# Kernel tuning notes

Measured on AMD Instinct MI355X. Metric: run time of the kernel, lower is better.

The kernel has to match this reference:

```python
import jax, jax.numpy as jnp
import numpy as np

D_MODEL = 768
N_HEADS = 8
HEAD_DIM = D_MODEL // N_HEADS  # 96


def setup_inputs() -> dict:
    key = jax.random.key(0)
    k1, k2, k3, k4, k5 = jax.random.split(key, 5)
    B, LQ, LK = 2, 4096, 4096
    hidden_states = jax.random.normal(k1, (B, LQ, D_MODEL), dtype=jnp.float32)
    key_value_states = jax.random.normal(k2, (B, LK, D_MODEL), dtype=jnp.float32)
    # learned projection params (initialized as eye in torch, but learned; use random here)
    Wq = jax.random.normal(k3, (D_MODEL, D_MODEL), dtype=jnp.float32) * 0.02
    Wk = jax.random.normal(k4, (D_MODEL, D_MODEL), dtype=jnp.float32) * 0.02
    Wv = jax.random.normal(k5, (D_MODEL, D_MODEL), dtype=jnp.float32) * 0.02
    return {"hidden_states": hidden_states, "key_value_states": key_value_states,
            "Wq": Wq, "Wk": Wk, "Wv": Wv}


def reference(hidden_states, key_value_states, Wq, Wk, Wv):
    B, LQ, _ = hidden_states.shape
    LK = key_value_states.shape[1]
    # linear projections (no bias)
    q = hidden_states @ Wq            # [B, LQ, D]
    k = key_value_states @ Wk         # [B, LK, D]
    v = key_value_states @ Wv         # [B, LK, D]
    # split heads: [B, H, L, d]
    def shape(x, L):
        return x.reshape(B, L, N_HEADS, HEAD_DIM).transpose(0, 2, 1, 3)
    q = shape(q, LQ) / jnp.sqrt(jnp.float32(HEAD_DIM))
    k = shape(k, LK)
    v = shape(v, LK)
    scores = jnp.einsum('bhqd,bhkd->bhqk', q, k)   # [B, H, LQ, LK]
    attn = jax.nn.softmax(scores, axis=-1)
    # dropout p=0.0 -> identity
    ctx = jnp.einsum('bhqk,bhkd->bhqd', attn, v)   # [B, H, LQ, d]
    context = ctx.transpose(0, 2, 1, 3).reshape(B, LQ, D_MODEL)
    return context
```

## Files before the change

kernel.cpp:

```cpp
#include <hip/hip_runtime.h>
#include <hip/hip_bf16.h>


typedef __bf16 bf16x8 __attribute__((ext_vector_type(8)));
typedef __bf16 bf16x4 __attribute__((ext_vector_type(4)));
typedef float  f32x4  __attribute__((ext_vector_type(4)));
typedef float  f32x16 __attribute__((ext_vector_type(16)));
typedef unsigned u32x4 __attribute__((ext_vector_type(4)));

#define DM   768
#define NH   8
#define HD   96
#define SEQ  4096
#define BATCH 2
#define WELEM (DM*DM)
#define XELEM (BATCH*SEQ*DM)

#define GLDS16(gp, lp) __builtin_amdgcn_global_load_lds( \
    (const __attribute__((address_space(1))) void*)(gp), \
    (__attribute__((address_space(3))) void*)(lp), 16, 0, 0)

__global__ __launch_bounds__(256) void transpose_w3(
    const float* __restrict__ Wq, const float* __restrict__ Wk, const float* __restrict__ Wv,
    __bf16* __restrict__ Tq, __bf16* __restrict__ Tk, __bf16* __restrict__ Tv)
{
    __shared__ __bf16 Ls[64][72];
    const int id = blockIdx.x;
    const int which = id / 144;
    const int tile = id - which * 144;
    const int ti = tile / 12, tj = tile % 12;
    const float* W = (which == 0) ? Wq : (which == 1) ? Wk : Wv;
    __bf16* T      = (which == 0) ? Tq : (which == 1) ? Tk : Tv;

    const int t = threadIdx.x;
    const int row = t >> 2, q4 = t & 3;
    const float* src = W + (size_t)(ti * 64 + row) * DM + tj * 64 + q4 * 16;
    float4 f0 = *reinterpret_cast<const float4*>(src);
    float4 f1 = *reinterpret_cast<const float4*>(src + 4);
    float4 f2 = *reinterpret_cast<const float4*>(src + 8);
    float4 f3 = *reinterpret_cast<const float4*>(src + 12);
    bf16x8 v0, v1;
    v0[0]=(__bf16)f0.x; v0[1]=(__bf16)f0.y; v0[2]=(__bf16)f0.z; v0[3]=(__bf16)f0.w;
    v0[4]=(__bf16)f1.x; v0[5]=(__bf16)f1.y; v0[6]=(__bf16)f1.z; v0[7]=(__bf16)f1.w;
    v1[0]=(__bf16)f2.x; v1[1]=(__bf16)f2.y; v1[2]=(__bf16)f2.z; v1[3]=(__bf16)f2.w;
    v1[4]=(__bf16)f3.x; v1[5]=(__bf16)f3.y; v1[6]=(__bf16)f3.z; v1[7]=(__bf16)f3.w;
    *reinterpret_cast<bf16x8*>(&Ls[row][q4 * 16])     = v0;
    *reinterpret_cast<bf16x8*>(&Ls[row][q4 * 16 + 8]) = v1;
    __syncthreads();
    #pragma unroll
    for (int j = 0; j < 2; ++j) {
        const int idx = t + j * 256;
        const int orow = idx >> 3, oc = idx & 7;
        bf16x8 o;
        #pragma unroll
        for (int e = 0; e < 8; ++e) o[e] = Ls[oc * 8 + e][orow];
        *reinterpret_cast<bf16x8*>(
            &T[(size_t)(tj * 64 + orow) * DM + ti * 64 + oc * 8]) = o;
    }
}

__global__ __launch_bounds__(256) void convert_x(
    const float* __restrict__ X0, const float* __restrict__ X1,
    __bf16* __restrict__ Y0, __bf16* __restrict__ Y1)
{
    const float* X = blockIdx.y ? X1 : X0;
    __bf16* Y      = blockIdx.y ? Y1 : Y0;
    const size_t i = ((size_t)blockIdx.x * 256 + threadIdx.x) * 8;
    float4 lo = *reinterpret_cast<const float4*>(X + i);
    float4 hi = *reinterpret_cast<const float4*>(X + i + 4);
    bf16x8 v;
    v[0]=(__bf16)lo.x; v[1]=(__bf16)lo.y; v[2]=(__bf16)lo.z; v[3]=(__bf16)lo.w;
    v[4]=(__bf16)hi.x; v[5]=(__bf16)hi.y; v[6]=(__bf16)hi.z; v[7]=(__bf16)hi.w;
    *reinterpret_cast<bf16x8*>(Y + i) = v;
}

__global__ __launch_bounds__(256, 2) void proj_all(
    const __bf16* __restrict__ Xh, const __bf16* __restrict__ Xkv,
    const __bf16* __restrict__ Wtq, const __bf16* __restrict__ Wtk,
    const __bf16* __restrict__ Wtv, __bf16* __restrict__ Yq,
    __bf16* __restrict__ Yk, __bf16* __restrict__ Yv, float qscale)
{
    __shared__ __bf16 As[2][128][64];
    __shared__ __bf16 Bs[2][128][64];

    const int t = threadIdx.x;
    const int l = t & 63;
    const int w = t >> 6;
    const int ln = l & 15, g = l >> 4;
    const int wm = w >> 1, wn = w & 1;

    const int id3 = blockIdx.x;
    const int xcd = id3 & 7;
    const int u = id3 >> 3;
    const int which = u % 3;
    const int c = u / 3;
    const int m0 = (xcd * 8 + c / 6) * 128;
    const int n0 = (c % 6) * 128;

    const __bf16* Xb = (which == 0) ? Xh : Xkv;
    const __bf16* Wt = (which == 0) ? Wtq : (which == 1) ? Wtk : Wtv;
    __bf16* Y        = (which == 0) ? Yq : (which == 1) ? Yk : Yv;
    const int mode   = (which == 2) ? 1 : 0;
    const float scale = (which == 0) ? qscale : 1.0f;

    size_t asrc[4], bsrc[4]; unsigned sdst[4];
    #pragma unroll
    for (int j = 0; j < 4; ++j) {
        const int cid = j * 256 + t;
        const int r = cid >> 3, cc = cid & 7, cs = cc ^ (r & 7);
        asrc[j] = (size_t)(m0 + r) * DM + cs * 8;
        bsrc[j] = (size_t)(n0 + r) * DM + cs * 8;
        sdst[j] = cid * 16;
    }

    f32x4 acc[4][4] = {};

    #pragma unroll
    for (int j = 0; j < 4; ++j) GLDS16(Xb + asrc[j], (char*)As + sdst[j]);
    #pragma unroll
    for (int j = 0; j < 4; ++j) GLDS16(Wt + bsrc[j], (char*)Bs + sdst[j]);
    __syncthreads();

    const int NKT = DM / 64;
    for (int kt = 0; kt < NKT; ++kt) {
        const int cur = kt & 1;
        if (kt + 1 < NKT) {
            const unsigned nb = (cur ^ 1) * 16384u;
            const size_t k0n = (size_t)(kt + 1) * 64;
            #pragma unroll
            for (int j = 0; j < 4; ++j) GLDS16(Xb + k0n + asrc[j], (char*)As + nb + sdst[j]);
            #pragma unroll
            for (int j = 0; j < 4; ++j) GLDS16(Wt + k0n + bsrc[j], (char*)Bs + nb + sdst[j]);
        }

        #pragma unroll
        for (int kk = 0; kk < 2; ++kk) {
            bf16x8 a[4], b[4];
            #pragma unroll
            for (int ms = 0; ms < 4; ++ms) {
                const int row = wm * 64 + ms * 16 + ln;
                const int slot = (kk * 4 + g) ^ (row & 7);
                a[ms] = *reinterpret_cast<const bf16x8*>(
                    (const char*)As + cur * 16384 + row * 128 + slot * 16);
            }
            #pragma unroll
            for (int ns = 0; ns < 4; ++ns) {
                const int row = wn * 64 + ns * 16 + ln;
                const int slot = (kk * 4 + g) ^ (row & 7);
                b[ns] = *reinterpret_cast<const bf16x8*>(
                    (const char*)Bs + cur * 16384 + row * 128 + slot * 16);
            }
            #pragma unroll
            for (int ms = 0; ms < 4; ++ms)
                #pragma unroll
                for (int ns = 0; ns < 4; ++ns)
                    acc[ms][ns] = __builtin_amdgcn_mfma_f32_16x16x32_bf16(
                        a[ms], b[ns], acc[ms][ns], 0, 0, 0);
        }
        __syncthreads();
    }

    #pragma unroll
    for (int ms = 0; ms < 4; ++ms) {
        #pragma unroll
        for (int ns = 0; ns < 4; ++ns) {
            const int col = n0 + wn * 64 + ns * 16 + ln;
            const int h = col / HD, d = col - h * HD;
            const int row_base = m0 + wm * 64 + ms * 16 + 4 * g;
            if (mode == 0) {
                #pragma unroll
                for (int r = 0; r < 4; ++r) {
                    const int row = row_base + r;
                    const int b_ = row >> 12, q = row & (SEQ - 1);
                    Y[(((size_t)(b_ * NH + h) * SEQ) + q) * HD + d] =
                        (__bf16)(acc[ms][ns][r] * scale);
                }
            } else {
                const int b_ = row_base >> 12, kq = row_base & (SEQ - 1);
                bf16x4 v;
                #pragma unroll
                for (int r = 0; r < 4; ++r) v[r] = (__bf16)acc[ms][ns][r];
                *reinterpret_cast<bf16x4*>(
                    &Y[((size_t)(b_ * NH + h) * HD + d) * SEQ + kq]) = v;
            }
        }
    }
}

__global__ __launch_bounds__(256, 2) void attn_kernel(
    const __bf16* __restrict__ Q, const __bf16* __restrict__ K,
    const __bf16* __restrict__ Vt, float* __restrict__ out)
{
    __shared__ __bf16 Ks[2][64][128];
    __shared__ __bf16 Vs[3][96][64];

    const int t_ = threadIdx.x;
    const int l = t_ & 63;
    const int w = t_ >> 6;
    const int lh = l >> 5;
    const int c31 = l & 31;

    const int swz = (blockIdx.x & 7) * 64 + (blockIdx.x >> 3);
    const int bh = swz >> 5;
    const int qb = swz & 31;
    const int b = bh >> 3, hd = bh & 7;
    const int q0 = qb * 128 + w * 32;

    const size_t base = (size_t)bh * SEQ * HD;
    const __bf16* Kg = K + base;
    const __bf16* Vg = Vt + base;

    size_t ksrc[4], vsrc[3];
    unsigned kdst[4], vdst[3];
    #pragma unroll
    for (int j = 0; j < 4; ++j) {
        const int cid = (w * 4 + j) * 64 + l;
        const int r = cid >> 4, cc = cid & 15;
        int cs = cc ^ (r & 7); if (cs >= 12) cs = 0;
        ksrc[j] = (size_t)r * HD + cs * 8;
        kdst[j] = (w * 4 + j) * 1024;
    }
    #pragma unroll
    for (int j = 0; j < 3; ++j) {
        const int cid = (w * 3 + j) * 64 + l;
        const int d = cid >> 3, cc = cid & 7;
        const int cs = cc ^ (d & 7);
        vsrc[j] = (size_t)d * SEQ + cs * 8;
        vdst[j] = (w * 3 + j) * 1024;
    }

    bf16x8 qf[6];
    #pragma unroll
    for (int st = 0; st < 6; ++st)
        qf[st] = *reinterpret_cast<const bf16x8*>(
            &Q[base + (size_t)(q0 + c31) * HD + st * 16 + 8 * lh]);

    f32x16 acc[3] = {};
    f32x16 sA0, sA1, sB0, sB1;
    float l_r = 0.f;
    int vcur = 0, vst = 2;
    f32x16 ZC = {};
    asm volatile("" : "+v"(ZC));

    auto STAGE = [&](int tile, int kp, int vbuf) {
        const size_t ko = (size_t)tile * 64 * HD;
        #pragma unroll
        for (int j = 0; j < 4; ++j)
            GLDS16(Kg + ko + ksrc[j], (char*)Ks + kp * 16384 + kdst[j]);
        const size_t vo = (size_t)tile * 64;
        #pragma unroll
        for (int j = 0; j < 3; ++j)
            GLDS16(Vg + vo + vsrc[j], (char*)Vs + vbuf * 12288 + vdst[j]);
    };

    auto QKT = [&](int pbuf, f32x16& S0, f32x16& S1) {
        #pragma unroll
        for (int st = 0; st < 6; ++st) {
            const int slot = (2 * st + lh) ^ (c31 & 7);
            bf16x8 ka0 = *reinterpret_cast<const bf16x8*>(
                (const char*)Ks + pbuf * 16384 + c31 * 256 + slot * 16);
            bf16x8 ka1 = *reinterpret_cast<const bf16x8*>(
                (const char*)Ks + pbuf * 16384 + (32 + c31) * 256 + slot * 16);
            S0 = __builtin_amdgcn_mfma_f32_32x32x16_bf16(ka0, qf[st],
                     st == 0 ? ZC : S0, 0, 0, 0);
            S1 = __builtin_amdgcn_mfma_f32_32x32x16_bf16(ka1, qf[st],
                     st == 0 ? ZC : S1, 0, 0, 0);
        }
    };

    auto SMPV = [&](f32x16& S0, f32x16& S1) {
        float p0 = 0.f, p1 = 0.f;
        #pragma unroll
        for (int r = 0; r < 16; ++r) {
            const float e0 = __builtin_amdgcn_exp2f(S0[r]);
            const float e1 = __builtin_amdgcn_exp2f(S1[r]);
            S0[r] = e0; S1[r] = e1; p0 += e0; p1 += e1;
        }
        l_r += p0 + p1;
        unsigned up[2][4][2];
        #pragma unroll
        for (int qd = 0; qd < 4; ++qd)
            #pragma unroll
            for (int j = 0; j < 2; ++j) {
                asm("v_cvt_pk_bf16_f32 %0, %1, %2"
                    : "=v"(up[0][qd][j])
                    : "v"(S0[4 * qd + 2 * j]), "v"(S0[4 * qd + 2 * j + 1]));
                asm("v_cvt_pk_bf16_f32 %0, %1, %2"
                    : "=v"(up[1][qd][j])
                    : "v"(S1[4 * qd + 2 * j]), "v"(S1[4 * qd + 2 * j + 1]));
            }
        const unsigned vbo = vcur * 12288;
        #pragma unroll
        for (int kc = 0; kc < 4; ++kc) {
            const int ks = kc >> 1, cp = kc & 1;
            unsigned x0 = up[ks][2 * cp][0],     x1 = up[ks][2 * cp][1];
            unsigned y0 = up[ks][2 * cp + 1][0], y1 = up[ks][2 * cp + 1][1];
            asm("v_permlane32_swap_b32 %0, %1" : "+v"(x0), "+v"(y0));
            asm("v_permlane32_swap_b32 %0, %1" : "+v"(x1), "+v"(y1));
            u32x4 pw; pw[0] = x0; pw[1] = x1; pw[2] = y0; pw[3] = y1;
            const bf16x8 pa = __builtin_bit_cast(bf16x8, pw);
            __builtin_amdgcn_s_setprio(1);
            #pragma unroll
            for (int dt = 0; dt < 3; ++dt) {
                const int dd = dt * 32 + c31;
                const int slot = (2 * kc + lh) ^ (dd & 7);
                bf16x8 vb = *reinterpret_cast<const bf16x8*>(
                    (const char*)Vs + vbo + dd * 128 + slot * 16);
                acc[dt] = __builtin_amdgcn_mfma_f32_32x32x16_bf16(pa, vb, acc[dt], 0, 0, 0);
            }
            __builtin_amdgcn_s_setprio(0);
        }
        vcur = (vcur == 2) ? 0 : vcur + 1;
        vst  = (vst  == 2) ? 0 : vst  + 1;
    };

    STAGE(0, 0, 0);
    __syncthreads();
    STAGE(1, 1, 1);
    QKT(0, sA0, sA1);

    const int NT = SEQ / 64;
    for (int u2 = 0; u2 < NT / 2; ++u2) {
        const int u = 2 * u2;
        __syncthreads();
        if (u + 2 < NT) STAGE(u + 2, 0, vst);
        QKT(1, sB0, sB1);
        SMPV(sA0, sA1);
        __syncthreads();
        if (u + 3 < NT) STAGE(u + 3, 1, vst);
        if (u + 2 < NT) QKT(0, sA0, sA1);
        SMPV(sB0, sB1);
    }

    {
        float ex = l_r;
        asm volatile("" : "+v"(ex));
        asm("v_permlane32_swap_b32 %0, %1" : "+v"(ex), "+v"(l_r));
        l_r += ex;
    }
    const float inv = 1.0f / l_r;
    #pragma unroll
    for (int r = 0; r < 16; ++r) {
        const int ql = (r & 3) + 8 * (r >> 2) + 4 * lh;
        const float ir = __shfl(inv, ql, 64);
        const int q = q0 + ql;
        float* dst = out + ((size_t)(b * SEQ + q)) * DM + hd * HD;
        #pragma unroll
        for (int dt = 0; dt < 3; ++dt)
            dst[dt * 32 + c31] = acc[dt][r] * ir;
    }
}

extern "C" void kernel_launch(void* const* d_in, const int* in_sizes, int n_in,
                              void* d_out, int out_size, void* d_ws, size_t ws_size,
                              hipStream_t stream) {
    const float* hidden = (const float*)d_in[0];
    const float* kv     = (const float*)d_in[1];
    const float* Wq     = (const float*)d_in[2];
    const float* Wk     = (const float*)d_in[3];
    const float* Wv     = (const float*)d_in[4];
    float* out = (float*)d_out;

    __bf16* Wt_q = (__bf16*)d_ws;
    __bf16* Wt_k = Wt_q + WELEM;
    __bf16* Wt_v = Wt_k + WELEM;
    __bf16* Qb   = Wt_v + WELEM;
    __bf16* Kb   = Qb + XELEM;
    __bf16* Vtb  = Kb + XELEM;

    __bf16* Xh_bf  = (__bf16*)d_out;
    __bf16* Xkv_bf = Xh_bf + XELEM;

    transpose_w3<<<432, 256, 0, stream>>>(Wq, Wk, Wv, Wt_q, Wt_k, Wt_v);
    convert_x<<<dim3(XELEM / 8 / 256, 2), 256, 0, stream>>>(hidden, kv, Xh_bf, Xkv_bf);

    const float qscale = 0.10206207261596575f * 1.4426950408889634f;
    proj_all<<<1152, 256, 0, stream>>>(Xh_bf, Xkv_bf, Wt_q, Wt_k, Wt_v,
                                       Qb, Kb, Vtb, qscale);

    attn_kernel<<<512, 256, 0, stream>>>(Qb, Kb, Vtb, out);
}
```

Before: 183.5 us.

## Split attention over two key halves and combine partial contexts in separate kernel

Splits the key/value sequence into two halves so the attention kernel launches twice as many blocks, each over 2048 keys, with smaller 32-key tiles and higher occupancy bounds. Each half writes unnormalized context and row sums. A new combine kernel adds the partials and normalizes. This raises parallelism across CUs but adds an extra fp32 context write/read round trip and a kernel launch. No max-subtraction is used, so summing the partials is valid.

```diff
diff --git a/kernel.cpp b/kernel.cpp
--- a/kernel.cpp
+++ b/kernel.cpp
@@ -187,12 +187,13 @@
     }
 }
 
-__global__ __launch_bounds__(256, 2) void attn_kernel(
+__global__ __launch_bounds__(256, 3) void attn_split(
     const __bf16* __restrict__ Q, const __bf16* __restrict__ K,
-    const __bf16* __restrict__ Vt, float* __restrict__ out)
-{
-    __shared__ __bf16 Ks[2][64][128];
-    __shared__ __bf16 Vs[3][96][64];
+    const __bf16* __restrict__ Vt, float* __restrict__ ctx0,
+    float* __restrict__ ctx1, float* __restrict__ lsum)
+{
+    __shared__ __bf16 Ks[2][32][128];
+    __shared__ __bf16 Vs[3][96][32];
 
     const int t_ = threadIdx.x;
     const int l = t_ & 63;
@@ -200,34 +201,34 @@
     const int lh = l >> 5;
     const int c31 = l & 31;
 
-    const int swz = (blockIdx.x & 7) * 64 + (blockIdx.x >> 3);
-    const int bh = swz >> 5;
-    const int qb = swz & 31;
+    const int swz = (blockIdx.x & 7) * 128 + (blockIdx.x >> 3);
+    const int bh = swz >> 6;
+    const int rem = swz & 63;
+    const int kh = rem >> 5;
+    const int qb = rem & 31;
     const int b = bh >> 3, hd = bh & 7;
     const int q0 = qb * 128 + w * 32;
 
     const size_t base = (size_t)bh * SEQ * HD;
-    const __bf16* Kg = K + base;
-    const __bf16* Vg = Vt + base;
-
-    size_t ksrc[4], vsrc[3];
-    unsigned kdst[4], vdst[3];
-    #pragma unroll
-    for (int j = 0; j < 4; ++j) {
-        const int cid = (w * 4 + j) * 64 + l;
+    const __bf16* Kg = K + base + (size_t)kh * 2048 * HD;
+    const __bf16* Vg = Vt + base + (size_t)kh * 2048;
+
+    size_t ksrc[2], vsrc[2];
+    unsigned kdst[2], vdst[2];
+    #pragma unroll
+    for (int j = 0; j < 2; ++j) {
+        const int cid = (w * 2 + j) * 64 + l;
         const int r = cid >> 4, cc = cid & 15;
         int cs = cc ^ (r & 7); if (cs >= 12) cs = 0;
         ksrc[j] = (size_t)r * HD + cs * 8;
-        kdst[j] = (w * 4 + j) * 1024;
-    }
-    #pragma unroll
-    for (int j = 0; j < 3; ++j) {
-        const int cid = (w * 3 + j) * 64 + l;
-        const int d = cid >> 3, cc = cid & 7;
-        const int cs = cc ^ (d & 7);
-        vsrc[j] = (size_t)d * SEQ + cs * 8;
-        vdst[j] = (w * 3 + j) * 1024;
-    }
+        kdst[j] = (w * 2 + j) * 1024;
+        const int vid = (w * 2 + j) * 64 + l;
+        const int d = vid >> 2, cc2 = vid & 3;
+        const int cs2 = (cc2 - (d >> 1)) & 3;
+        vsrc[j] = (size_t)(d < 96 ? d : 0) * SEQ + cs2 * 8;
+        vdst[j] = (w * 2 + j) * 1024;
+    }
+    const bool vdo[2] = { (w * 2 + 0) < 6, (w * 2 + 1) < 6 };
 
     bf16x8 qf[6];
     #pragma unroll
@@ -236,65 +237,54 @@
             &Q[base + (size_t)(q0 + c31) * HD + st * 16 + 8 * lh]);
 
     f32x16 acc[3] = {};
-    f32x16 sA0, sA1, sB0, sB1;
+    f32x16 sA, sB;
     float l_r = 0.f;
     int vcur = 0, vst = 2;
-    f32x16 ZC = {};
-    asm volatile("" : "+v"(ZC));
 
     auto STAGE = [&](int tile, int kp, int vbuf) {
-        const size_t ko = (size_t)tile * 64 * HD;
-        #pragma unroll
-        for (int j = 0; j < 4; ++j)
-            GLDS16(Kg + ko + ksrc[j], (char*)Ks + kp * 16384 + kdst[j]);
-        const size_t vo = (size_t)tile * 64;
-        #pragma unroll
-        for (int j = 0; j < 3; ++j)
-            GLDS16(Vg + vo + vsrc[j], (char*)Vs + vbuf * 12288 + vdst[j]);
+        const size_t ko = (size_t)tile * 32 * HD;
+        #pragma unroll
+        for (int j = 0; j < 2; ++j)
+            GLDS16(Kg + ko + ksrc[j], (char*)Ks + kp * 8192 + kdst[j]);
+        const size_t vo = (size_t)tile * 32;
+        #pragma unroll
+        for (int j = 0; j < 2; ++j)
+            if (vdo[j])
+                GLDS16(Vg + vo + vsrc[j], (char*)Vs + vbuf * 6144 + vdst[j]);
     };
 
-    auto QKT = [&](int pbuf, f32x16& S0, f32x16& S1) {
+    auto QKT = [&](int pbuf, f32x16& S) {
+        S = (f32x16){};
         #pragma unroll
         for (int st = 0; st < 6; ++st) {
             const int slot = (2 * st + lh) ^ (c31 & 7);
-            bf16x8 ka0 = *reinterpret_cast<const bf16x8*>(
-                (const char*)Ks + pbuf * 16384 + c31 * 256 + slot * 16);
-            bf16x8 ka1 = *reinterpret_cast<const bf16x8*>(
-                (const char*)Ks + pbuf * 16384 + (32 + c31) * 256 + slot * 16);
-            S0 = __builtin_amdgcn_mfma_f32_32x32x16_bf16(ka0, qf[st],
-                     st == 0 ? ZC : S0, 0, 0, 0);
-            S1 = __builtin_amdgcn_mfma_f32_32x32x16_bf16(ka1, qf[st],
-                     st == 0 ? ZC : S1, 0, 0, 0);
+            bf16x8 ka = *reinterpret_cast<const bf16x8*>(
+                (const char*)Ks + pbuf * 8192 + c31 * 256 + slot * 16);
+            S = __builtin_amdgcn_mfma_f32_32x32x16_bf16(ka, qf[st], S, 0, 0, 0);
         }
     };
 
-    auto SMPV = [&](f32x16& S0, f32x16& S1) {
-        float p0 = 0.f, p1 = 0.f;
+    auto SMPV = [&](f32x16& S) {
+        float ps = 0.f;
         #pragma unroll
         for (int r = 0; r < 16; ++r) {
-            const float e0 = __builtin_amdgcn_exp2f(S0[r]);
-            const float e1 = __builtin_amdgcn_exp2f(S1[r]);
-            S0[r] = e0; S1[r] = e1; p0 += e0; p1 += e1;
-        }
-        l_r += p0 + p1;
-        unsigned up[2][4][2];
+            const float e = __builtin_amdgcn_exp2f(S[r]);
+            S[r] = e; ps += e;
+        }
+        l_r += ps;
+        unsigned up[4][2];
         #pragma unroll
         for (int qd = 0; qd < 4; ++qd)
             #pragma unroll
-            for (int j = 0; j < 2; ++j) {
+            for (int j = 0; j < 2; ++j)
                 asm("v_cvt_pk_bf16_f32 %0, %1, %2"
-                    : "=v"(up[0][qd][j])
-                    : "v"(S0[4 * qd + 2 * j]), "v"(S0[4 * qd + 2 * j + 1]));
-                asm("v_cvt_pk_bf16_f32 %0, %1, %2"
-                    : "=v"(up[1][qd][j])
-                    : "v"(S1[4 * qd + 2 * j]), "v"(S1[4 * qd + 2 * j + 1]));
-            }
-        const unsigned vbo = vcur * 12288;
-        #pragma unroll
-        for (int kc = 0; kc < 4; ++kc) {
-            const int ks = kc >> 1, cp = kc & 1;
-            unsigned x0 = up[ks][2 * cp][0],     x1 = up[ks][2 * cp][1];
-            unsigned y0 = up[ks][2 * cp + 1][0], y1 = up[ks][2 * cp + 1][1];
+                    : "=v"(up[qd][j])
+                    : "v"(S[4 * qd + 2 * j]), "v"(S[4 * qd + 2 * j + 1]));
+        const unsigned vbo = vcur * 6144;
+        #pragma unroll
+        for (int kc = 0; kc < 2; ++kc) {
+            unsigned x0 = up[2 * kc][0],     x1 = up[2 * kc][1];
+            unsigned y0 = up[2 * kc + 1][0], y1 = up[2 * kc + 1][1];
             asm("v_permlane32_swap_b32 %0, %1" : "+v"(x0), "+v"(y0));
             asm("v_permlane32_swap_b32 %0, %1" : "+v"(x1), "+v"(y1));
             u32x4 pw; pw[0] = x0; pw[1] = x1; pw[2] = y0; pw[3] = y1;
@@ -303,9 +293,9 @@
             #pragma unroll
             for (int dt = 0; dt < 3; ++dt) {
                 const int dd = dt * 32 + c31;
-                const int slot = (2 * kc + lh) ^ (dd & 7);
+                const int slot = ((2 * kc + lh) + (dd >> 1)) & 3;
                 bf16x8 vb = *reinterpret_cast<const bf16x8*>(
-                    (const char*)Vs + vbo + dd * 128 + slot * 16);
+                    (const char*)Vs + vbo + dd * 64 + slot * 16);
                 acc[dt] = __builtin_amdgcn_mfma_f32_32x32x16_bf16(pa, vb, acc[dt], 0, 0, 0);
             }
             __builtin_amdgcn_s_setprio(0);
@@ -317,19 +307,19 @@
     STAGE(0, 0, 0);
     __syncthreads();
     STAGE(1, 1, 1);
-    QKT(0, sA0, sA1);
-
-    const int NT = SEQ / 64;
+    QKT(0, sA);
+
+    const int NT = 2048 / 32;
     for (int u2 = 0; u2 < NT / 2; ++u2) {
         const int u = 2 * u2;
         __syncthreads();
         if (u + 2 < NT) STAGE(u + 2, 0, vst);
-        QKT(1, sB0, sB1);
-        SMPV(sA0, sA1);
+        QKT(1, sB);
+        SMPV(sA);
         __syncthreads();
         if (u + 3 < NT) STAGE(u + 3, 1, vst);
-        if (u + 2 < NT) QKT(0, sA0, sA1);
-        SMPV(sB0, sB1);
+        if (u + 2 < NT) QKT(0, sA);
+        SMPV(sB);
     }
 
     {
@@ -338,17 +328,39 @@
         asm("v_permlane32_swap_b32 %0, %1" : "+v"(ex), "+v"(l_r));
         l_r += ex;
     }
-    const float inv = 1.0f / l_r;
+    float* ctx = kh ? ctx1 : ctx0;
     #pragma unroll
     for (int r = 0; r < 16; ++r) {
         const int ql = (r & 3) + 8 * (r >> 2) + 4 * lh;
-        const float ir = __shfl(inv, ql, 64);
         const int q = q0 + ql;
-        float* dst = out + ((size_t)(b * SEQ + q)) * DM + hd * HD;
+        float* dst = ctx + ((size_t)(b * SEQ + q)) * DM + hd * HD;
         #pragma unroll
         for (int dt = 0; dt < 3; ++dt)
-            dst[dt * 32 + c31] = acc[dt][r] * ir;
-    }
+            dst[dt * 32 + c31] = acc[dt][r];
+    }
+    if (lh == 0)
+        lsum[kh * 65536 + bh * SEQ + q0 + c31] = l_r;
+}
+
+__global__ __launch_bounds__(256) void combine2(
+    const float* __restrict__ ctx1, const float* __restrict__ lsum,
+    float* __restrict__ outc)
+{
+    const size_t e4 = (size_t)blockIdx.x * 256 + threadIdx.x;
+    const size_t e = e4 * 4;
+    const int row = (int)(e / DM);
+    const int dfull = (int)(e - (size_t)row * DM);
+    const int hd = dfull / HD;
+    const int b = row >> 12, q = row & (SEQ - 1);
+    const int bh = b * NH + hd;
+    const float lv = lsum[bh * SEQ + q] + lsum[65536 + bh * SEQ + q];
+    const float inv = 1.0f / lv;
+    float4 c0 = *reinterpret_cast<const float4*>(outc + e);
+    float4 c1 = *reinterpret_cast<const float4*>(ctx1 + e);
+    float4 o;
+    o.x = (c0.x + c1.x) * inv; o.y = (c0.y + c1.y) * inv;
+    o.z = (c0.z + c1.z) * inv; o.w = (c0.w + c1.w) * inv;
+    *reinterpret_cast<float4*>(outc + e) = o;
 }
 
 extern "C" void kernel_launch(void* const* d_in, const int* in_sizes, int n_in,
@@ -367,6 +379,8 @@
     __bf16* Qb   = Wt_v + WELEM;
     __bf16* Kb   = Qb + XELEM;
     __bf16* Vtb  = Kb + XELEM;
+    float*  ctx1 = (float*)(Vtb + XELEM);
+    float*  lsum = ctx1 + XELEM;
 
     __bf16* Xh_bf  = (__bf16*)d_out;
     __bf16* Xkv_bf = Xh_bf + XELEM;
@@ -378,5 +392,6 @@
     proj_all<<<1152, 256, 0, stream>>>(Xh_bf, Xkv_bf, Wt_q, Wt_k, Wt_v,
                                        Qb, Kb, Vtb, qscale);
 
-    attn_kernel<<<512, 256, 0, stream>>>(Qb, Kb, Vtb, out);
-}
+    attn_split<<<1024, 256, 0, stream>>>(Qb, Kb, Vtb, out, ctx1, lsum);
+    combine2<<<XELEM / 4 / 256, 256, 0, stream>>>(ctx1, lsum, out);
+}
```

After: 207.4 us. +13.0%, slower.
